# Kernel tuning notes

Hardware: AMD Instinct MI355X
Metric: run time of the kernel (lower is better)

## Reference

```python
import jax, jax.numpy as jnp
import numpy as np
from jax import lax

B, C, H, W = 8, 64, 256, 256
WSIZES = [8, 8]
DRATES = [1, 2]
SHIFT = True
CS = C // len(WSIZES)          # split channels = 32
SCALE = CS ** (-0.5)
EPS = 1e-6


def _ln2d(x, w, b):
    # channel-wise LayerNorm over dim 1 (biased variance), per LayerNormFunction
    mu = x.mean(1, keepdims=True)
    var = ((x - mu) ** 2).mean(1, keepdims=True)
    y = (x - mu) / jnp.sqrt(var + EPS)
    return w[None, :, None, None] * y + b[None, :, None, None]


def _conv1d(x, w, pad, dil):
    # x: [b, ci, L], w: [co, ci, k]
    return lax.conv_general_dilated(x, w, (1,), ((pad, pad),), rhs_dilation=(dil,),
                                    dimension_numbers=('NCH', 'OIH', 'NCH'))


def _eca(x, w1, w2, w3, wc):
    # x: [b,c,h,w] -> channel attention [b,c,1,1]
    y = x.mean((2, 3))[:, None, :]                      # [b,1,c]
    y1 = _conv1d(y, w1, 1, 1)
    y2 = _conv1d(y, w2, 2, 2)
    y3 = _conv1d(y, w3, 4, 4)
    y = _conv1d(jnp.concatenate([y1, y2, y3], axis=1), wc, 1, 1)  # [b,1,c]
    return jax.nn.sigmoid(jnp.transpose(y, (0, 2, 1))[..., None])  # [b,c,1,1]


def _conv1x1(x, w):
    # w: [co, ci]
    return jnp.einsum('bchw,oc->bohw', x, w)


def _win(x, ws):
    # [b,c,H,W] -> [(b nh nw), ws*ws, c]
    b, c, h, w = x.shape
    nh, nw = h // ws, w // ws
    x = x.reshape(b, c, nh, ws, nw, ws).transpose(0, 2, 4, 3, 5, 1)
    return x.reshape(b * nh * nw, ws * ws, c)


def _unwin(x, b, nh, nw, ws):
    c = x.shape[-1]
    x = x.reshape(b, nh, nw, ws, ws, c).transpose(0, 5, 1, 3, 2, 4)
    return x.reshape(b, c, nh * ws, nw * ws)


def setup_inputs() -> dict:
    key = jax.random.key(0)
    ks = jax.random.split(key, 16)
    g = lambda k, shape: jax.random.normal(k, shape, jnp.float32) * 0.02
    return {
        'x0': jax.random.normal(ks[0], (B, C, H, W), jnp.float32),
        'ln_w': jnp.ones((C,), jnp.float32),
        'ln_b': jnp.zeros((C,), jnp.float32),
        'dw_w': g(ks[1], (C, 1, 3, 3)),
        'dw_b': jnp.zeros((C,), jnp.float32),
        'eca_w1': g(ks[2], (1, 1, 3)),
        'eca_w2': g(ks[3], (1, 1, 3)),
        'eca_w3': g(ks[4], (1, 1, 3)),
        'eca_wc': g(ks[5], (1, 3, 3)),
        'wq': g(ks[6], (C, C)),
        'wk': g(ks[7], (C, C)),
        'wv': g(ks[8], (C, C)),
        'down_w': g(ks[9], (CS, 1, 2, 2)),
        'down_b': jnp.zeros((CS,), jnp.float32),
        'sa_w': g(ks[10], (1, C)),
        'sa_b': jnp.zeros((1,), jnp.float32),
        'po_w': g(ks[11], (C, C)),
        'po_b': jnp.zeros((C,), jnp.float32),
    }


def reference(x0, ln_w, ln_b, dw_w, dw_b, eca_w1, eca_w2, eca_w3, eca_wc,
              wq, wk, wv, down_w, down_b, sa_w, sa_b, po_w, po_b):
    b, c, h, w = x0.shape
    x = _ln2d(x0, ln_w, ln_b)
    # depthwise 3x3
    x1 = lax.conv_general_dilated(x, dw_w, (1, 1), ((1, 1), (1, 1)),
                                  feature_group_count=c,
                                  dimension_numbers=('NCHW', 'OIHW', 'NCHW'))
    x1 = x1 + dw_b[None, :, None, None]
    ca = _eca(x1, eca_w1, eca_w2, eca_w3, eca_wc)
    vs = jnp.split(_conv1x1(x, wv) * ca, len(WSIZES), axis=1)
    qs = jnp.split(_conv1x1(x, wq), len(WSIZES), axis=1)
    ks_ = jnp.split(_conv1x1(x, wk), len(WSIZES), axis=1)

    ys = []
    for idx in range(len(WSIZES)):
        ws = WSIZES[idx]
        ds = ws // DRATES[idx]
        q = qs[idx]
        if SHIFT:
            q = jnp.roll(q, (-ws // 2, -ws // 2), (2, 3))
        q = _win(q, ws)
        if DRATES[idx] != 1:
            # depthwise 2x2 stride-2 downsample of k, v
            def down(t):
                t = lax.conv_general_dilated(t, down_w, (2, 2), 'VALID',
                                             feature_group_count=CS,
                                             dimension_numbers=('NCHW', 'OIHW', 'NCHW'))
                return t + down_b[None, :, None, None]
            k = down(ks_[idx])
            v = down(vs[idx])
            if SHIFT:
                k = jnp.roll(k, (-ds // 2, -ds // 2), (2, 3))
                v = jnp.roll(v, (-ds // 2, -ds // 2), (2, 3))
            k = _win(k, ds)
            v = _win(v, ds)
        else:
            k, v = ks_[idx], vs[idx]
            if SHIFT:
                k = jnp.roll(k, (-ws // 2, -ws // 2), (2, 3))
                v = jnp.roll(v, (-ws // 2, -ws // 2), (2, 3))
            k = _win(k, ws)
            v = _win(v, ws)
        atn = jax.nn.softmax(jnp.einsum('nqc,nkc->nqk', q, k) * SCALE, axis=-1)
        y_ = jnp.einsum('nqk,nkc->nqc', atn, v)
        y_ = _unwin(y_, b, h // ws, w // ws, ws)
        if SHIFT:
            y_ = jnp.roll(y_, (ws // 2, ws // 2), (2, 3))
        ys.append(y_)

    y = jnp.concatenate(ys, axis=1)
    x1m = jax.nn.sigmoid(_conv1x1(y, sa_w) + sa_b[None, :, None, None]) * x1
    y = _conv1x1(y + x1m, po_w) + po_b[None, :, None, None]
    return y + x0
```

## Files before the change

### kernel.cpp

```cpp
#include <hip/hip_runtime.h>
#include <hip/hip_bf16.h>

using bf16 = __hip_bfloat16;

constexpr int B = 8, C = 64, H = 256, W = 256;
constexpr int HWs = H * W;
constexpr int NPIX = B * H * W;
constexpr long long NELEM = (long long)B * C * H * W;
constexpr int CS = 32;
constexpr int Hd = 128, Wd = 128;
constexpr int HWd = Hd * Wd;
constexpr int NDOWN = B * CS * HWd;
constexpr float EPS = 1e-6f;
constexpr float SCALE = 0.17677669529663687f;

typedef __attribute__((ext_vector_type(8))) short short8v;
typedef __attribute__((ext_vector_type(8))) unsigned short ushort8v;
typedef __attribute__((ext_vector_type(4))) unsigned short ushort4v;
typedef __attribute__((ext_vector_type(4))) float f32x4;

__device__ __forceinline__ float b2f(bf16 v) { return __bfloat162float(v); }
__device__ __forceinline__ bf16 f2b(float v) { return __float2bfloat16(v); }
__device__ __forceinline__ unsigned short f2bu(float v) {
  bf16 t = __float2bfloat16(v);
  unsigned short u;
  __builtin_memcpy(&u, &t, 2);
  return u;
}
__device__ __forceinline__ float bu2f(unsigned short u) {
  bf16 t;
  __builtin_memcpy(&t, &u, 2);
  return __bfloat162float(t);
}
__device__ __forceinline__ short8v pack2(ushort4v a, ushort4v b) {
  short8v r;
  r[0] = (short)a[0]; r[1] = (short)a[1]; r[2] = (short)a[2]; r[3] = (short)a[3];
  r[4] = (short)b[0]; r[5] = (short)b[1]; r[6] = (short)b[2]; r[7] = (short)b[3];
  return r;
}

__global__ __launch_bounds__(256) void qkv_ln_kernel(
    const float* __restrict__ x0, const float* __restrict__ lnw,
    const float* __restrict__ lnb, const float* __restrict__ wq,
    const float* __restrict__ wk, const float* __restrict__ wv,
    unsigned short* __restrict__ xo, unsigned short* __restrict__ q0,
    unsigned short* __restrict__ q1, unsigned short* __restrict__ k0,
    unsigned short* __restrict__ v0, unsigned short* __restrict__ ksp,
    unsigned short* __restrict__ vsp) {
  __shared__ unsigned short zs[4][16 * 80];
  int lane = threadIdx.x & 63, wid = threadIdx.x >> 6;
  int lr = lane & 15, lg = lane >> 4;
  short8v aq[4][2], ak[4][2], av[4][2];
#pragma unroll
  for (int mt = 0; mt < 4; ++mt)
#pragma unroll
    for (int ks = 0; ks < 2; ++ks) {
      int rowoff = (mt * 16 + lr) * 64 + ks * 32 + lg * 4;
      short8v tq, tk, tv;
#pragma unroll
      for (int j = 0; j < 8; ++j) {
        int kj = (j & 3) + 16 * (j >> 2);
        tq[j] = (short)f2bu(wq[rowoff + kj]);
        tk[j] = (short)f2bu(wk[rowoff + kj]);
        tv[j] = (short)f2bu(wv[rowoff + kj]);
      }
      aq[mt][ks] = tq; ak[mt][ks] = tk; av[mt][ks] = tv;
    }
  float lwv[16], lbv[16];
#pragma unroll
  for (int ks = 0; ks < 2; ++ks)
#pragma unroll
    for (int j = 0; j < 8; ++j) {
      int c = ks * 32 + lg * 4 + (j & 3) + 16 * (j >> 2);
      lwv[ks * 8 + j] = lnw[c];
      lbv[ks * 8 + j] = lnb[c];
    }
  unsigned short* slab = &zs[wid][0];
  const int NT = NPIX / 16;
  for (int t = blockIdx.x * 4 + wid; t < NT; t += gridDim.x * 4) {
    int p0 = t * 16;
    int b = p0 >> 16;
    int hw0 = p0 & (HWs - 1);
    const float* xp = x0 + (size_t)b * C * HWs + hw0 + lr;
    float xv[16];
#pragma unroll
    for (int ks = 0; ks < 2; ++ks)
#pragma unroll
      for (int j = 0; j < 8; ++j) {
        int c = ks * 32 + lg * 4 + (j & 3) + 16 * (j >> 2);
        xv[ks * 8 + j] = xp[(size_t)c * HWs];
      }
    float s = 0.f, s2 = 0.f;
#pragma unroll
    for (int i = 0; i < 16; ++i) { s += xv[i]; s2 += xv[i] * xv[i]; }
    s += __shfl_xor(s, 16, 64); s += __shfl_xor(s, 32, 64);
    s2 += __shfl_xor(s2, 16, 64); s2 += __shfl_xor(s2, 32, 64);
    float mu = s * (1.f / 64);
    float var = s2 * (1.f / 64) - mu * mu;
    float rstd = rsqrtf(var + EPS);
    short8v bx[2];
#pragma unroll
    for (int ks = 0; ks < 2; ++ks)
#pragma unroll
      for (int j = 0; j < 8; ++j) {
        float xn = lwv[ks * 8 + j] * ((xv[ks * 8 + j] - mu) * rstd) + lbv[ks * 8 + j];
        bx[ks][j] = (short)f2bu(xn);
      }
    int r = hw0 >> 8, col0 = hw0 & 255;
    int rr = (r - 4) & 255;
    int tokr = (rr & 7) * 8;
    int wrow = b * 1024 + (rr >> 3) * 32;
    int px = lane & 15, ch4 = lane >> 4;
    int ccw = (col0 + px - 4) & 255;
    size_t wb = (size_t)(wrow + (ccw >> 3)) * 2048 + (size_t)(tokr + (ccw & 7)) * 32 + ch4 * 8;
    int chs = 32 + (lane & 31), ph = lane >> 5;
    f32x4 zero = {0.f, 0.f, 0.f, 0.f};
#pragma unroll
    for (int ks = 0; ks < 2; ++ks)
#pragma unroll
      for (int j = 0; j < 8; ++j) {
        int c = ks * 32 + lg * 4 + (j & 3) + 16 * (j >> 2);
        slab[lr * 80 + c] = (unsigned short)bx[ks][j];
      }
    {
      int ch = lane;
      ushort8v d0, d1;
#pragma unroll
      for (int j2 = 0; j2 < 8; ++j2) {
        d0[j2] = slab[j2 * 80 + ch];
        d1[j2] = slab[(8 + j2) * 80 + ch];
      }
      size_t sb = ((size_t)b * 64 + ch) * HWs + hw0;
      *(ushort8v*)(xo + sb) = d0;
      *(ushort8v*)(xo + sb + 8) = d1;
    }
    {
      f32x4 acc[4];
#pragma unroll
      for (int mt = 0; mt < 4; ++mt) {
        acc[mt] = __builtin_amdgcn_mfma_f32_16x16x32_bf16(aq[mt][0], bx[0], zero, 0, 0, 0);
        acc[mt] = __builtin_amdgcn_mfma_f32_16x16x32_bf16(aq[mt][1], bx[1], acc[mt], 0, 0, 0);
      }
#pragma unroll
      for (int mt = 0; mt < 4; ++mt)
#pragma unroll
        for (int i = 0; i < 4; ++i)
          slab[lr * 80 + mt * 16 + lg * 4 + i] = f2bu(acc[mt][i]);
      ushort8v dq0 = *(const ushort8v*)&slab[px * 80 + ch4 * 8];
      ushort8v dq1 = *(const ushort8v*)&slab[px * 80 + 32 + ch4 * 8];
      *(ushort8v*)(q0 + wb) = dq0;
      *(ushort8v*)(q1 + wb) = dq1;
    }
    {
      f32x4 acc[4];
#pragma unroll
      for (int mt = 0; mt < 4; ++mt) {
        acc[mt] = __builtin_amdgcn_mfma_f32_16x16x32_bf16(ak[mt][0], bx[0], zero, 0, 0, 0);
        acc[mt] = __builtin_amdgcn_mfma_f32_16x16x32_bf16(ak[mt][1], bx[1], acc[mt], 0, 0, 0);
      }
#pragma unroll
      for (int mt = 0; mt < 4; ++mt)
#pragma unroll
        for (int i = 0; i < 4; ++i)
          slab[lr * 80 + mt * 16 + lg * 4 + i] = f2bu(acc[mt][i]);
      ushort8v dk = *(const ushort8v*)&slab[px * 80 + ch4 * 8];
      *(ushort8v*)(k0 + wb) = dk;
      ushort8v dks;
#pragma unroll
      for (int j2 = 0; j2 < 8; ++j2) dks[j2] = slab[(ph * 8 + j2) * 80 + chs];
      size_t sb = ((size_t)b * 32 + (chs - 32)) * HWs + hw0 + ph * 8;
      *(ushort8v*)(ksp + sb) = dks;
    }
    {
      f32x4 acc[4];
#pragma unroll
      for (int mt = 0; mt < 4; ++mt) {
        acc[mt] = __builtin_amdgcn_mfma_f32_16x16x32_bf16(av[mt][0], bx[0], zero, 0, 0, 0);
        acc[mt] = __builtin_amdgcn_mfma_f32_16x16x32_bf16(av[mt][1], bx[1], acc[mt], 0, 0, 0);
      }
#pragma unroll
      for (int mt = 0; mt < 4; ++mt)
#pragma unroll
        for (int i = 0; i < 4; ++i)
          slab[lr * 80 + mt * 16 + lg * 4 + i] = f2bu(acc[mt][i]);
      ushort8v dv = *(const ushort8v*)&slab[px * 80 + ch4 * 8];
      *(ushort8v*)(v0 + wb) = dv;
      ushort8v dvs;
#pragma unroll
      for (int j2 = 0; j2 < 8; ++j2) dvs[j2] = slab[(ph * 8 + j2) * 80 + chs];
      size_t sb = ((size_t)b * 32 + (chs - 32)) * HWs + hw0 + ph * 8;
      *(ushort8v*)(vsp + sb) = dvs;
    }
  }
}

__global__ __launch_bounds__(256) void dw_kernel(
    const unsigned short* __restrict__ x, const float* __restrict__ dww,
    const float* __restrict__ dwb, unsigned short* __restrict__ x1,
    float* __restrict__ pool) {
  int tid = threadIdx.x;
  int tx = tid & 15, ty = tid >> 4;
  int h = blockIdx.x * 16 + ty;
  int c = blockIdx.y, b = blockIdx.z;
  const unsigned short* xp = x + ((size_t)b * C + c) * HWs;
  float kk[9];
#pragma unroll
  for (int i = 0; i < 9; ++i) kk[i] = dww[c * 9 + i];
  int w0 = tx * 16;
  float acc[16];
  float bias = dwb[c];
#pragma unroll
  for (int i = 0; i < 16; ++i) acc[i] = bias;
#pragma unroll
  for (int dr = 0; dr < 3; ++dr) {
    int hh = h + dr - 1;
    if (hh < 0 || hh >= H) continue;
    const unsigned short* rp = xp + hh * W;
    ushort8v r0 = *(const ushort8v*)(rp + w0);
    ushort8v r1 = *(const ushort8v*)(rp + w0 + 8);
    float p[18];
    p[0] = (w0 > 0) ? bu2f(rp[w0 - 1]) : 0.f;
    p[17] = (w0 + 16 < W) ? bu2f(rp[w0 + 16]) : 0.f;
#pragma unroll
    for (int i = 0; i < 8; ++i) { p[1 + i] = bu2f(r0[i]); p[9 + i] = bu2f(r1[i]); }
    float k0 = kk[dr * 3], k1 = kk[dr * 3 + 1], k2 = kk[dr * 3 + 2];
#pragma unroll
    for (int i = 0; i < 16; ++i)
      acc[i] += k0 * p[i] + k1 * p[i + 1] + k2 * p[i + 2];
  }
  ushort8v o0, o1;
  float s = 0.f;
#pragma unroll
  for (int i = 0; i < 8; ++i) { o0[i] = f2bu(acc[i]); o1[i] = f2bu(acc[i + 8]); }
#pragma unroll
  for (int i = 0; i < 16; ++i) s += acc[i];
  size_t ob = ((size_t)b * C + c) * HWs + h * W + w0;
  *(ushort8v*)(x1 + ob) = o0;
  *(ushort8v*)(x1 + ob + 8) = o1;
#pragma unroll
  for (int off = 32; off > 0; off >>= 1) s += __shfl_down(s, off, 64);
  __shared__ float red[4];
  if ((tid & 63) == 0) red[tid >> 6] = s;
  __syncthreads();
  if (tid == 0) atomicAdd(&pool[b * C + c], red[0] + red[1] + red[2] + red[3]);
}

__global__ __launch_bounds__(512) void eca_kernel(
    const float* __restrict__ pool, const float* __restrict__ w1,
    const float* __restrict__ w2, const float* __restrict__ w3,
    const float* __restrict__ wc, float* __restrict__ ca) {
  int tid = threadIdx.x;
  int b = tid >> 6, c = tid & 63;
  __shared__ float m[8][64], t1[8][64], t2[8][64], t3[8][64];
  m[b][c] = pool[tid] * (1.f / HWs);
  __syncthreads();
  auto gm = [&](int cc) -> float { return (cc >= 0 && cc < 64) ? m[b][cc] : 0.f; };
  t1[b][c] = w1[0] * gm(c - 1) + w1[1] * gm(c) + w1[2] * gm(c + 1);
  t2[b][c] = w2[0] * gm(c - 2) + w2[1] * gm(c) + w2[2] * gm(c + 2);
  t3[b][c] = w3[0] * gm(c - 4) + w3[1] * gm(c) + w3[2] * gm(c + 4);
  __syncthreads();
  auto g1 = [&](int cc) -> float { return (cc >= 0 && cc < 64) ? t1[b][cc] : 0.f; };
  auto g2 = [&](int cc) -> float { return (cc >= 0 && cc < 64) ? t2[b][cc] : 0.f; };
  auto g3 = [&](int cc) -> float { return (cc >= 0 && cc < 64) ? t3[b][cc] : 0.f; };
  float z = 0.f;
#pragma unroll
  for (int k = 0; k < 3; ++k) {
    z += wc[0 * 3 + k] * g1(c + k - 1);
    z += wc[1 * 3 + k] * g2(c + k - 1);
    z += wc[2 * 3 + k] * g3(c + k - 1);
  }
  ca[tid] = 1.f / (1.f + __expf(-z));
}

__global__ __launch_bounds__(256) void down_kernel(
    const unsigned short* __restrict__ ksp, const unsigned short* __restrict__ vsp,
    const float* __restrict__ dw, const float* __restrict__ db,
    unsigned short* __restrict__ kdw, unsigned short* __restrict__ vdw) {
  int t = blockIdx.x * 256 + threadIdx.x;
  int wxd = t & 31, i = (t >> 5) & 127, c = (t >> 12) & 31, b = t >> 17;
  const unsigned short* kp = ksp + ((size_t)b * 32 + c) * HWs;
  const unsigned short* vp = vsp + ((size_t)b * 32 + c) * HWs;
  float w00 = dw[c * 4], w01 = dw[c * 4 + 1], w10 = dw[c * 4 + 2], w11 = dw[c * 4 + 3];
  float bias = db[c];
  int rowa = (2 * i) * W, rowb = rowa + W;
  int c0a = (8 * wxd + 4) & 255, c0b = (8 * wxd + 8) & 255;
  ushort4v ka0 = *(const ushort4v*)(kp + rowa + c0a);
  ushort4v ka1 = *(const ushort4v*)(kp + rowa + c0b);
  ushort4v kb0 = *(const ushort4v*)(kp + rowb + c0a);
  ushort4v kb1 = *(const ushort4v*)(kp + rowb + c0b);
  ushort4v va0 = *(const ushort4v*)(vp + rowa + c0a);
  ushort4v va1 = *(const ushort4v*)(vp + rowa + c0b);
  ushort4v vb0 = *(const ushort4v*)(vp + rowb + c0a);
  ushort4v vb1 = *(const ushort4v*)(vp + rowb + c0b);
  int rr = (i - 2) & 127;
  size_t winb = ((size_t)(b * 1024 + (rr >> 2) * 32 + wxd)) * 512;
  int tokrow = (rr & 3) * 4;
  ushort4v hk, hv;
#pragma unroll
  for (int tx = 0; tx < 4; ++tx) {
    float k00, k01, k10, k11, v00, v01, v10, v11;
    if (tx < 2) {
      k00 = bu2f(ka0[2 * tx]); k01 = bu2f(ka0[2 * tx + 1]);
      k10 = bu2f(kb0[2 * tx]); k11 = bu2f(kb0[2 * tx + 1]);
      v00 = bu2f(va0[2 * tx]); v01 = bu2f(va0[2 * tx + 1]);
      v10 = bu2f(vb0[2 * tx]); v11 = bu2f(vb0[2 * tx + 1]);
    } else {
      k00 = bu2f(ka1[2 * (tx - 2)]); k01 = bu2f(ka1[2 * (tx - 2) + 1]);
      k10 = bu2f(kb1[2 * (tx - 2)]); k11 = bu2f(kb1[2 * (tx - 2) + 1]);
      v00 = bu2f(va1[2 * (tx - 2)]); v01 = bu2f(va1[2 * (tx - 2) + 1]);
      v10 = bu2f(vb1[2 * (tx - 2)]); v11 = bu2f(vb1[2 * (tx - 2) + 1]);
    }
    hk[tx] = f2bu(w00 * k00 + w01 * k01 + w10 * k10 + w11 * k11 + bias);
    hv[tx] = f2bu(w00 * v00 + w01 * v01 + w10 * v10 + w11 * v11 + bias);
  }
  *(ushort4v*)(vdw + winb + (size_t)c * 16 + tokrow) = hv;
#pragma unroll
  for (int tx = 0; tx < 4; ++tx)
    kdw[winb + (size_t)(tokrow + tx) * 32 + c] = hk[tx];
}

__global__ __launch_bounds__(256) void attn0_kernel(
    const unsigned short* __restrict__ q0, const unsigned short* __restrict__ k0,
    const unsigned short* __restrict__ v0, const float* __restrict__ ca,
    unsigned short* __restrict__ y) {
  __shared__ unsigned short zs[4][32][72];
  int lane = threadIdx.x & 63, wid = threadIdx.x >> 6;
  int lr = lane & 15, lg = lane >> 4;
  int widx = blockIdx.x * 4 + wid;
  int b = widx >> 10, wy = (widx >> 5) & 31, wx = widx & 31;
  unsigned short* zw = &zs[wid][0][0];
  float cav[8];
#pragma unroll
  for (int mt = 0; mt < 2; ++mt)
#pragma unroll
    for (int r2 = 0; r2 < 4; ++r2)
      cav[mt * 4 + r2] = ca[b * 64 + mt * 16 + lg * 4 + r2];
  {
    const unsigned short* vp = v0 + (size_t)widx * 2048 + (size_t)lane * 32;
#pragma unroll
    for (int j2 = 0; j2 < 4; ++j2) {
      ushort8v vv = *(const ushort8v*)(vp + j2 * 8);
#pragma unroll
      for (int i = 0; i < 8; ++i) zw[(j2 * 8 + i) * 72 + lane] = vv[i];
    }
  }
  const unsigned short* kw = k0 + (size_t)widx * 2048;
  const unsigned short* qw = q0 + (size_t)widx * 2048;
  short8v kf[4], qf[4];
#pragma unroll
  for (int kt = 0; kt < 4; ++kt) {
    ushort4v a = *(const ushort4v*)(kw + (kt * 16 + lr) * 32 + lg * 4);
    ushort4v b2 = *(const ushort4v*)(kw + (kt * 16 + lr) * 32 + lg * 4 + 16);
    kf[kt] = pack2(a, b2);
  }
#pragma unroll
  for (int qt = 0; qt < 4; ++qt) {
    ushort4v a = *(const ushort4v*)(qw + (qt * 16 + lr) * 32 + lg * 4);
    ushort4v b2 = *(const ushort4v*)(qw + (qt * 16 + lr) * 32 + lg * 4 + 16);
    qf[qt] = pack2(a, b2);
  }
  __syncthreads();
  short8v va[2][2];
#pragma unroll
  for (int mt = 0; mt < 2; ++mt)
#pragma unroll
    for (int ck = 0; ck < 2; ++ck) {
      ushort4v a = *(const ushort4v*)&zw[(mt * 16 + lr) * 72 + ck * 32 + lg * 4];
      ushort4v b2 = *(const ushort4v*)&zw[(mt * 16 + lr) * 72 + ck * 32 + lg * 4 + 16];
      va[mt][ck] = pack2(a, b2);
    }
  f32x4 zero = {0.f, 0.f, 0.f, 0.f};
#pragma unroll
  for (int qt = 0; qt < 4; ++qt) {
    f32x4 st[4];
#pragma unroll
    for (int kt = 0; kt < 4; ++kt)
      st[kt] = __builtin_amdgcn_mfma_f32_16x16x32_bf16(kf[kt], qf[qt], zero, 0, 0, 0);
    float mx = -1e30f;
#pragma unroll
    for (int kt = 0; kt < 4; ++kt)
#pragma unroll
      for (int r2 = 0; r2 < 4; ++r2) mx = fmaxf(mx, st[kt][r2]);
    mx = fmaxf(mx, __shfl_xor(mx, 16, 64));
    mx = fmaxf(mx, __shfl_xor(mx, 32, 64));
    float sum = 0.f;
#pragma unroll
    for (int kt = 0; kt < 4; ++kt)
#pragma unroll
      for (int r2 = 0; r2 < 4; ++r2) {
        float e = __expf(SCALE * (st[kt][r2] - mx));
        st[kt][r2] = e;
        sum += e;
      }
    sum += __shfl_xor(sum, 16, 64);
    sum += __shfl_xor(sum, 32, 64);
    float inv = 1.f / sum;
    short8v pb[2];
#pragma unroll
    for (int ck = 0; ck < 2; ++ck)
#pragma unroll
      for (int j = 0; j < 8; ++j)
        pb[ck][j] = (short)f2bu(st[ck * 2 + (j >> 2)][j & 3]);
#pragma unroll
    for (int mt = 0; mt < 2; ++mt) {
      f32x4 yt = __builtin_amdgcn_mfma_f32_16x16x32_bf16(va[mt][0], pb[0], zero, 0, 0, 0);
      yt = __builtin_amdgcn_mfma_f32_16x16x32_bf16(va[mt][1], pb[1], yt, 0, 0, 0);
#pragma unroll
      for (int r2 = 0; r2 < 4; ++r2)
        zw[(mt * 16 + lg * 4 + r2) * 72 + qt * 16 + lr] = f2bu(yt[r2] * inv * cav[mt * 4 + r2]);
    }
  }
  __syncthreads();
  int ch = lane & 31, rh = lane >> 5;
  size_t ybase = ((size_t)b * C + ch) * HWs;
  int c1 = wx * 8 + 4, c2 = (wx * 8 + 8) & 255;
#pragma unroll
  for (int k2 = 0; k2 < 4; ++k2) {
    int row = rh * 4 + k2;
    ushort8v t8 = *(const ushort8v*)&zw[ch * 72 + row * 8];
    int r = (wy * 8 + row + 4) & 255;
    ushort4v lo, hi;
#pragma unroll
    for (int i = 0; i < 4; ++i) { lo[i] = t8[i]; hi[i] = t8[4 + i]; }
    *(ushort4v*)(y + ybase + r * W + c1) = lo;
    *(ushort4v*)(y + ybase + r * W + c2) = hi;
  }
}

__global__ __launch_bounds__(256) void attn1_kernel(
    const unsigned short* __restrict__ q1, const unsigned short* __restrict__ kdw,
    const unsigned short* __restrict__ vdw, const float* __restrict__ ca,
    unsigned short* __restrict__ y) {
  __shared__ unsigned short zs[4][32][72];
  int lane = threadIdx.x & 63, wid = threadIdx.x >> 6;
  int lr = lane & 15, lg = lane >> 4;
  int widx = blockIdx.x * 4 + wid;
  int b = widx >> 10, wy = (widx >> 5) & 31, wx = widx & 31;
  unsigned short* zw = &zs[wid][0][0];
  float cav[8];
#pragma unroll
  for (int mt = 0; mt < 2; ++mt)
#pragma unroll
    for (int r2 = 0; r2 < 4; ++r2)
      cav[mt * 4 + r2] = ca[b * 64 + 32 + mt * 16 + lg * 4 + r2];
  short8v kfr;
  {
    ushort4v a = *(const ushort4v*)(kdw + (size_t)widx * 512 + lr * 32 + lg * 4);
    ushort4v b2 = *(const ushort4v*)(kdw + (size_t)widx * 512 + lr * 32 + lg * 4 + 16);
    kfr = pack2(a, b2);
  }
  short8v va[2];
#pragma unroll
  for (int mt = 0; mt < 2; ++mt) {
    ushort4v a = *(const ushort4v*)(vdw + (size_t)widx * 512 + (mt * 16 + lr) * 16 + lg * 4);
    short8v t;
#pragma unroll
    for (int i = 0; i < 4; ++i) { t[i] = (short)a[i]; t[4 + i] = 0; }
    va[mt] = t;
  }
  const unsigned short* qw = q1 + (size_t)widx * 2048;
  short8v qf[4];
#pragma unroll
  for (int qt = 0; qt < 4; ++qt) {
    ushort4v a = *(const ushort4v*)(qw + (qt * 16 + lr) * 32 + lg * 4);
    ushort4v b2 = *(const ushort4v*)(qw + (qt * 16 + lr) * 32 + lg * 4 + 16);
    qf[qt] = pack2(a, b2);
  }
  f32x4 zero = {0.f, 0.f, 0.f, 0.f};
#pragma unroll
  for (int qt = 0; qt < 4; ++qt) {
    f32x4 st = __builtin_amdgcn_mfma_f32_16x16x32_bf16(kfr, qf[qt], zero, 0, 0, 0);
    float mx = fmaxf(fmaxf(st[0], st[1]), fmaxf(st[2], st[3]));
    mx = fmaxf(mx, __shfl_xor(mx, 16, 64));
    mx = fmaxf(mx, __shfl_xor(mx, 32, 64));
    float sum = 0.f;
#pragma unroll
    for (int r2 = 0; r2 < 4; ++r2) {
      float e = __expf(SCALE * (st[r2] - mx));
      st[r2] = e;
      sum += e;
    }
    sum += __shfl_xor(sum, 16, 64);
    sum += __shfl_xor(sum, 32, 64);
    float inv = 1.f / sum;
    short8v pb;
#pragma unroll
    for (int j = 0; j < 4; ++j) { pb[j] = (short)f2bu(st[j]); pb[4 + j] = 0; }
#pragma unroll
    for (int mt = 0; mt < 2; ++mt) {
      f32x4 yt = __builtin_amdgcn_mfma_f32_16x16x32_bf16(va[mt], pb, zero, 0, 0, 0);
#pragma unroll
      for (int r2 = 0; r2 < 4; ++r2)
        zw[(mt * 16 + lg * 4 + r2) * 72 + qt * 16 + lr] = f2bu(yt[r2] * inv * cav[mt * 4 + r2]);
    }
  }
  __syncthreads();
  int ch = lane & 31, rh = lane >> 5;
  size_t ybase = ((size_t)b * C + 32 + ch) * HWs;
  int c1 = wx * 8 + 4, c2 = (wx * 8 + 8) & 255;
#pragma unroll
  for (int k2 = 0; k2 < 4; ++k2) {
    int row = rh * 4 + k2;
    ushort8v t8 = *(const ushort8v*)&zw[ch * 72 + row * 8];
    int r = (wy * 8 + row + 4) & 255;
    ushort4v lo, hi;
#pragma unroll
    for (int i = 0; i < 4; ++i) { lo[i] = t8[i]; hi[i] = t8[4 + i]; }
    *(ushort4v*)(y + ybase + r * W + c1) = lo;
    *(ushort4v*)(y + ybase + r * W + c2) = hi;
  }
}

__global__ __launch_bounds__(256) void final_mfma_kernel(
    const unsigned short* __restrict__ y, const unsigned short* __restrict__ x1,
    const float* __restrict__ x0, const float* __restrict__ sa_w,
    const float* __restrict__ sa_b, const float* __restrict__ po_w,
    const float* __restrict__ po_b, float* __restrict__ out) {
  __shared__ unsigned short zs[64][72];
  __shared__ float part[4][64];
  __shared__ float sgs[64];
  int tid = threadIdx.x;
  int lane = tid & 63, wid = tid >> 6;
  int lr = lane & 15, lg = lane >> 4;
  short8v ap[4][2];
#pragma unroll
  for (int mt = 0; mt < 4; ++mt)
#pragma unroll
    for (int ks = 0; ks < 2; ++ks) {
      int rowoff = (mt * 16 + lr) * 64 + ks * 32 + lg * 4;
      short8v tt;
#pragma unroll
      for (int j = 0; j < 8; ++j) {
        int kj = (j & 3) + 16 * (j >> 2);
        tt[j] = (short)f2bu(po_w[rowoff + kj]);
      }
      ap[mt][ks] = tt;
    }
  int cc = tid >> 2, qx = (tid & 3) * 16;
  const int NBLK = NPIX / 64;
  for (int blk = blockIdx.x; blk < NBLK; blk += gridDim.x) {
    int p0 = blk * 64;
    int b = p0 >> 16, hw0 = p0 & (HWs - 1);
    size_t rbase = (size_t)b * C * HWs + (size_t)cc * HWs + hw0 + qx;
    ushort8v y0 = *(const ushort8v*)(y + rbase);
    ushort8v y1 = *(const ushort8v*)(y + rbase + 8);
    ushort8v a0 = *(const ushort8v*)(x1 + rbase);
    ushort8v a1 = *(const ushort8v*)(x1 + rbase + 8);
    *(ushort8v*)&zs[cc][qx] = y0;
    *(ushort8v*)&zs[cc][qx + 8] = y1;
    __syncthreads();
    {
      int p = tid & 63, qr = tid >> 6;
      float s = 0.f;
#pragma unroll
      for (int c2 = 0; c2 < 16; ++c2)
        s += sa_w[qr * 16 + c2] * bu2f(zs[qr * 16 + c2][p]);
      part[qr][p] = s;
    }
    __syncthreads();
    if (tid < 64) {
      float sd = part[0][tid] + part[1][tid] + part[2][tid] + part[3][tid] + sa_b[0];
      sgs[tid] = 1.f / (1.f + __expf(-sd));
    }
    __syncthreads();
    {
      ushort8v z0, z1;
#pragma unroll
      for (int i = 0; i < 8; ++i) {
        z0[i] = f2bu(bu2f(y0[i]) + sgs[qx + i] * bu2f(a0[i]));
        z1[i] = f2bu(bu2f(y1[i]) + sgs[qx + 8 + i] * bu2f(a1[i]));
      }
      *(ushort8v*)&zs[cc][qx] = z0;
      *(ushort8v*)&zs[cc][qx + 8] = z1;
    }
    __syncthreads();
    short8v bz[2];
#pragma unroll
    for (int ks = 0; ks < 2; ++ks) {
      short8v tt;
#pragma unroll
      for (int j = 0; j < 8; ++j) {
        int c2 = ks * 32 + lg * 4 + (j & 3) + 16 * (j >> 2);
        tt[j] = (short)zs[c2][wid * 16 + lr];
      }
      bz[ks] = tt;
    }
    f32x4 zero = {0.f, 0.f, 0.f, 0.f};
    f32x4 acc[4];
#pragma unroll
    for (int mt = 0; mt < 4; ++mt) {
      acc[mt] = __builtin_amdgcn_mfma_f32_16x16x32_bf16(ap[mt][0], bz[0], zero, 0, 0, 0);
      acc[mt] = __builtin_amdgcn_mfma_f32_16x16x32_bf16(ap[mt][1], bz[1], acc[mt], 0, 0, 0);
    }
    size_t pbase = (size_t)b * C * HWs + hw0 + wid * 16 + lr;
#pragma unroll
    for (int mt = 0; mt < 4; ++mt)
#pragma unroll
      for (int i = 0; i < 4; ++i) {
        int o = mt * 16 + lg * 4 + i;
        out[pbase + (size_t)o * HWs] = acc[mt][i] + po_b[o] + x0[pbase + (size_t)o * HWs];
      }
    __syncthreads();
  }
}

extern "C" void kernel_launch(void* const* d_in, const int* in_sizes, int n_in,
                              void* d_out, int out_size, void* d_ws, size_t ws_size,
                              hipStream_t stream) {
  const float* x0    = (const float*)d_in[0];
  const float* ln_w  = (const float*)d_in[1];
  const float* ln_b  = (const float*)d_in[2];
  const float* dw_w  = (const float*)d_in[3];
  const float* dw_b  = (const float*)d_in[4];
  const float* ew1   = (const float*)d_in[5];
  const float* ew2   = (const float*)d_in[6];
  const float* ew3   = (const float*)d_in[7];
  const float* ewc   = (const float*)d_in[8];
  const float* wq    = (const float*)d_in[9];
  const float* wk    = (const float*)d_in[10];
  const float* wv    = (const float*)d_in[11];
  const float* dwn_w = (const float*)d_in[12];
  const float* dwn_b = (const float*)d_in[13];
  const float* sa_w  = (const float*)d_in[14];
  const float* sa_b  = (const float*)d_in[15];
  const float* po_w  = (const float*)d_in[16];
  const float* po_b  = (const float*)d_in[17];
  float* out = (float*)d_out;

  char* ws = (char*)d_ws;
  const size_t NB = (size_t)NELEM * sizeof(bf16);
  const size_t NH = NB / 2;
  const size_t NDB = (size_t)NDOWN * sizeof(bf16);
  bf16* xbuf  = (bf16*)(ws);
  bf16* x1buf = (bf16*)(ws + NB);
  unsigned short* q0b  = (unsigned short*)(ws + 2 * NB);
  unsigned short* q1b  = (unsigned short*)(ws + 2 * NB + NH);
  unsigned short* k0b  = (unsigned short*)(ws + 3 * NB);
  unsigned short* v0b  = (unsigned short*)(ws + 3 * NB + NH);
  unsigned short* kspb = (unsigned short*)(ws + 4 * NB);
  unsigned short* vspb = (unsigned short*)(ws + 4 * NB + NH);
  unsigned short* kdwb = (unsigned short*)(ws + 5 * NB);
  unsigned short* vdwb = (unsigned short*)(ws + 5 * NB + NDB);
  float* pool = (float*)(ws + 5 * NB + 2 * NDB);
  float* cabuf = pool + B * C;
  bf16* ybuf = xbuf;

  hipMemsetAsync(pool, 0, B * C * sizeof(float), stream);
  qkv_ln_kernel<<<2048, 256, 0, stream>>>(x0, ln_w, ln_b, wq, wk, wv,
                                          (unsigned short*)xbuf, q0b, q1b, k0b, v0b,
                                          kspb, vspb);
  dw_kernel<<<dim3(16, C, B), 256, 0, stream>>>((const unsigned short*)xbuf, dw_w, dw_b,
                                                (unsigned short*)x1buf, pool);
  eca_kernel<<<1, 512, 0, stream>>>(pool, ew1, ew2, ew3, ewc, cabuf);
  down_kernel<<<4096, 256, 0, stream>>>(kspb, vspb, dwn_w, dwn_b, kdwb, vdwb);
  attn0_kernel<<<2048, 256, 0, stream>>>(q0b, k0b, v0b, cabuf, (unsigned short*)ybuf);
  attn1_kernel<<<2048, 256, 0, stream>>>(q1b, kdwb, vdwb, cabuf, (unsigned short*)ybuf);
  final_mfma_kernel<<<2048, 256, 0, stream>>>((const unsigned short*)ybuf,
                                              (const unsigned short*)x1buf, x0,
                                              sa_w, sa_b, po_w, po_b, out);
}
```

Before: 407.4 us.

## Restructure QKV kernel into 64-pixel segments and coalesce attention output stores

The QKV/LayerNorm kernel stops using a grid-stride loop over 16-pixel tiles. Each wave now handles one 64-pixel segment, loading weight fragments one matrix at a time instead of holding all three, and stages outputs through two LDS buffers so that windowed and channel-major stores become wider and more contiguous. In both attention kernels the output store is now done cooperatively by the whole block across its four adjacent windows, giving 16-byte stores instead of split 8-byte ones. The aim is better global-store coalescing and lower register pressure, at the cost of more LDS traffic. The new kernel also relies on the launch grid covering exactly NPIX/64 segments.

```diff
diff --git a/kernel.cpp b/kernel.cpp
--- a/kernel.cpp
+++ b/kernel.cpp
@@ -47,25 +47,17 @@
     unsigned short* __restrict__ q1, unsigned short* __restrict__ k0,
     unsigned short* __restrict__ v0, unsigned short* __restrict__ ksp,
     unsigned short* __restrict__ vsp) {
-  __shared__ unsigned short zs[4][16 * 80];
+  __shared__ unsigned short sA[4][2560];
+  __shared__ unsigned short sB[4][2560];
   int lane = threadIdx.x & 63, wid = threadIdx.x >> 6;
   int lr = lane & 15, lg = lane >> 4;
-  short8v aq[4][2], ak[4][2], av[4][2];
-#pragma unroll
-  for (int mt = 0; mt < 4; ++mt)
-#pragma unroll
-    for (int ks = 0; ks < 2; ++ks) {
-      int rowoff = (mt * 16 + lr) * 64 + ks * 32 + lg * 4;
-      short8v tq, tk, tv;
-#pragma unroll
-      for (int j = 0; j < 8; ++j) {
-        int kj = (j & 3) + 16 * (j >> 2);
-        tq[j] = (short)f2bu(wq[rowoff + kj]);
-        tk[j] = (short)f2bu(wk[rowoff + kj]);
-        tv[j] = (short)f2bu(wv[rowoff + kj]);
-      }
-      aq[mt][ks] = tq; ak[mt][ks] = tk; av[mt][ks] = tv;
-    }
+  unsigned short* A = &sA[wid][0];
+  unsigned short* Bs = &sB[wid][0];
+  int seg = blockIdx.x * 4 + wid;
+  int p0 = seg * 64;
+  int b = p0 >> 16;
+  int hw0 = p0 & (HWs - 1);
+  int r = hw0 >> 8, col0 = hw0 & 255;
   float lwv[16], lbv[16];
 #pragma unroll
   for (int ks = 0; ks < 2; ++ks)
@@ -75,13 +67,10 @@
       lwv[ks * 8 + j] = lnw[c];
       lbv[ks * 8 + j] = lnb[c];
     }
-  unsigned short* slab = &zs[wid][0];
-  const int NT = NPIX / 16;
-  for (int t = blockIdx.x * 4 + wid; t < NT; t += gridDim.x * 4) {
-    int p0 = t * 16;
-    int b = p0 >> 16;
-    int hw0 = p0 & (HWs - 1);
-    const float* xp = x0 + (size_t)b * C * HWs + hw0 + lr;
+  short8v bx[4][2];
+#pragma unroll
+  for (int st = 0; st < 4; ++st) {
+    const float* xp = x0 + (size_t)b * C * HWs + hw0 + st * 16 + lr;
     float xv[16];
 #pragma unroll
     for (int ks = 0; ks < 2; ++ks)
@@ -98,98 +87,150 @@
     float mu = s * (1.f / 64);
     float var = s2 * (1.f / 64) - mu * mu;
     float rstd = rsqrtf(var + EPS);
-    short8v bx[2];
 #pragma unroll
     for (int ks = 0; ks < 2; ++ks)
 #pragma unroll
       for (int j = 0; j < 8; ++j) {
         float xn = lwv[ks * 8 + j] * ((xv[ks * 8 + j] - mu) * rstd) + lbv[ks * 8 + j];
-        bx[ks][j] = (short)f2bu(xn);
-      }
-    int r = hw0 >> 8, col0 = hw0 & 255;
-    int rr = (r - 4) & 255;
-    int tokr = (rr & 7) * 8;
-    int wrow = b * 1024 + (rr >> 3) * 32;
-    int px = lane & 15, ch4 = lane >> 4;
-    int ccw = (col0 + px - 4) & 255;
-    size_t wb = (size_t)(wrow + (ccw >> 3)) * 2048 + (size_t)(tokr + (ccw & 7)) * 32 + ch4 * 8;
-    int chs = 32 + (lane & 31), ph = lane >> 5;
-    f32x4 zero = {0.f, 0.f, 0.f, 0.f};
-#pragma unroll
-    for (int ks = 0; ks < 2; ++ks)
+        bx[st][ks][j] = (short)f2bu(xn);
+      }
+  }
+  int rr = (r - 4) & 255;
+  int tokr = (rr & 7) * 8;
+  int wrow = b * 1024 + (rr >> 3) * 32;
+  auto win_store = [&](const unsigned short* src, unsigned short* dst) {
+#pragma unroll
+    for (int i = 0; i < 4; ++i) {
+      int g = i * 4 + (lane >> 4);
+      int tl = (lane >> 2) & 3, ch8 = lane & 3;
+      int px = g * 4 + tl;
+      int ccw = (col0 + px - 4) & 255;
+      size_t wb = (size_t)(wrow + (ccw >> 3)) * 2048 +
+                  (size_t)(tokr + (ccw & 7)) * 32 + ch8 * 8;
+      ushort8v d = *(const ushort8v*)(src + px * 40 + ch8 * 8);
+      *(ushort8v*)(dst + wb) = d;
+    }
+  };
+  auto load_wfrag = [&](const float* wsrc, short8v wf[4][2]) {
+#pragma unroll
+    for (int mt = 0; mt < 4; ++mt)
+#pragma unroll
+      for (int ks = 0; ks < 2; ++ks) {
+        int rowoff = (mt * 16 + lr) * 64 + ks * 32 + lg * 4;
+        short8v t;
+#pragma unroll
+        for (int j = 0; j < 8; ++j) {
+          int kj = (j & 3) + 16 * (j >> 2);
+          t[j] = (short)f2bu(wsrc[rowoff + kj]);
+        }
+        wf[mt][ks] = t;
+      }
+  };
+  f32x4 zero = {0.f, 0.f, 0.f, 0.f};
+#pragma unroll
+  for (int half = 0; half < 2; ++half) {
+#pragma unroll
+    for (int st = 0; st < 4; ++st) {
+      int px = st * 16 + lr;
 #pragma unroll
       for (int j = 0; j < 8; ++j) {
-        int c = ks * 32 + lg * 4 + (j & 3) + 16 * (j >> 2);
-        slab[lr * 80 + c] = (unsigned short)bx[ks][j];
-      }
-    {
-      int ch = lane;
-      ushort8v d0, d1;
-#pragma unroll
-      for (int j2 = 0; j2 < 8; ++j2) {
-        d0[j2] = slab[j2 * 80 + ch];
-        d1[j2] = slab[(8 + j2) * 80 + ch];
-      }
-      size_t sb = ((size_t)b * 64 + ch) * HWs + hw0;
-      *(ushort8v*)(xo + sb) = d0;
-      *(ushort8v*)(xo + sb + 8) = d1;
-    }
-    {
+        int c = lg * 4 + (j & 3) + 16 * (j >> 2);
+        Bs[c * 80 + px] = (unsigned short)bx[st][half][j];
+      }
+    }
+#pragma unroll
+    for (int i = 0; i < 4; ++i) {
+      int ch = i * 8 + (lane >> 3), pxg = lane & 7;
+      ushort8v d = *(const ushort8v*)(Bs + ch * 80 + pxg * 8);
+      *(ushort8v*)(xo + ((size_t)b * 64 + half * 32 + ch) * HWs + hw0 + pxg * 8) = d;
+    }
+  }
+  {
+    short8v wf[4][2];
+    load_wfrag(wq, wf);
+#pragma unroll
+    for (int st = 0; st < 4; ++st) {
       f32x4 acc[4];
 #pragma unroll
       for (int mt = 0; mt < 4; ++mt) {
-        acc[mt] = __builtin_amdgcn_mfma_f32_16x16x32_bf16(aq[mt][0], bx[0], zero, 0, 0, 0);
-        acc[mt] = __builtin_amdgcn_mfma_f32_16x16x32_bf16(aq[mt][1], bx[1], acc[mt], 0, 0, 0);
-      }
-#pragma unroll
-      for (int mt = 0; mt < 4; ++mt)
+        acc[mt] = __builtin_amdgcn_mfma_f32_16x16x32_bf16(wf[mt][0], bx[st][0], zero, 0, 0, 0);
+        acc[mt] = __builtin_amdgcn_mfma_f32_16x16x32_bf16(wf[mt][1], bx[st][1], acc[mt], 0, 0, 0);
+      }
+      int px = st * 16 + lr;
+#pragma unroll
+      for (int mt = 0; mt < 2; ++mt)
 #pragma unroll
         for (int i = 0; i < 4; ++i)
-          slab[lr * 80 + mt * 16 + lg * 4 + i] = f2bu(acc[mt][i]);
-      ushort8v dq0 = *(const ushort8v*)&slab[px * 80 + ch4 * 8];
-      ushort8v dq1 = *(const ushort8v*)&slab[px * 80 + 32 + ch4 * 8];
-      *(ushort8v*)(q0 + wb) = dq0;
-      *(ushort8v*)(q1 + wb) = dq1;
-    }
-    {
+          A[px * 40 + mt * 16 + lg * 4 + i] = f2bu(acc[mt][i]);
+#pragma unroll
+      for (int mt = 2; mt < 4; ++mt)
+#pragma unroll
+        for (int i = 0; i < 4; ++i)
+          Bs[px * 40 + (mt - 2) * 16 + lg * 4 + i] = f2bu(acc[mt][i]);
+    }
+    win_store(A, q0);
+    win_store(Bs, q1);
+  }
+  {
+    short8v wf[4][2];
+    load_wfrag(wk, wf);
+#pragma unroll
+    for (int st = 0; st < 4; ++st) {
       f32x4 acc[4];
 #pragma unroll
       for (int mt = 0; mt < 4; ++mt) {
-        acc[mt] = __builtin_amdgcn_mfma_f32_16x16x32_bf16(ak[mt][0], bx[0], zero, 0, 0, 0);
-        acc[mt] = __builtin_amdgcn_mfma_f32_16x16x32_bf16(ak[mt][1], bx[1], acc[mt], 0, 0, 0);
-      }
-#pragma unroll
-      for (int mt = 0; mt < 4; ++mt)
+        acc[mt] = __builtin_amdgcn_mfma_f32_16x16x32_bf16(wf[mt][0], bx[st][0], zero, 0, 0, 0);
+        acc[mt] = __builtin_amdgcn_mfma_f32_16x16x32_bf16(wf[mt][1], bx[st][1], acc[mt], 0, 0, 0);
+      }
+      int px = st * 16 + lr;
+#pragma unroll
+      for (int mt = 0; mt < 2; ++mt)
 #pragma unroll
         for (int i = 0; i < 4; ++i)
-          slab[lr * 80 + mt * 16 + lg * 4 + i] = f2bu(acc[mt][i]);
-      ushort8v dk = *(const ushort8v*)&slab[px * 80 + ch4 * 8];
-      *(ushort8v*)(k0 + wb) = dk;
-      ushort8v dks;
-#pragma unroll
-      for (int j2 = 0; j2 < 8; ++j2) dks[j2] = slab[(ph * 8 + j2) * 80 + chs];
-      size_t sb = ((size_t)b * 32 + (chs - 32)) * HWs + hw0 + ph * 8;
-      *(ushort8v*)(ksp + sb) = dks;
-    }
-    {
+          A[px * 40 + mt * 16 + lg * 4 + i] = f2bu(acc[mt][i]);
+#pragma unroll
+      for (int mt = 2; mt < 4; ++mt)
+#pragma unroll
+        for (int i = 0; i < 4; ++i)
+          Bs[((mt - 2) * 16 + lg * 4 + i) * 80 + px] = f2bu(acc[mt][i]);
+    }
+    win_store(A, k0);
+#pragma unroll
+    for (int i = 0; i < 4; ++i) {
+      int ch = i * 8 + (lane >> 3), pxg = lane & 7;
+      ushort8v d = *(const ushort8v*)(Bs + ch * 80 + pxg * 8);
+      *(ushort8v*)(ksp + ((size_t)b * 32 + ch) * HWs + hw0 + pxg * 8) = d;
+    }
+  }
+  {
+    short8v wf[4][2];
+    load_wfrag(wv, wf);
+#pragma unroll
+    for (int st = 0; st < 4; ++st) {
       f32x4 acc[4];
 #pragma unroll
       for (int mt = 0; mt < 4; ++mt) {
-        acc[mt] = __builtin_amdgcn_mfma_f32_16x16x32_bf16(av[mt][0], bx[0], zero, 0, 0, 0);
-        acc[mt] = __builtin_amdgcn_mfma_f32_16x16x32_bf16(av[mt][1], bx[1], acc[mt], 0, 0, 0);
-      }
-#pragma unroll
-      for (int mt = 0; mt < 4; ++mt)
+        acc[mt] = __builtin_amdgcn_mfma_f32_16x16x32_bf16(wf[mt][0], bx[st][0], zero, 0, 0, 0);
+        acc[mt] = __builtin_amdgcn_mfma_f32_16x16x32_bf16(wf[mt][1], bx[st][1], acc[mt], 0, 0, 0);
+      }
+      int px = st * 16 + lr;
+#pragma unroll
+      for (int mt = 0; mt < 2; ++mt)
 #pragma unroll
         for (int i = 0; i < 4; ++i)
-          slab[lr * 80 + mt * 16 + lg * 4 + i] = f2bu(acc[mt][i]);
-      ushort8v dv = *(const ushort8v*)&slab[px * 80 + ch4 * 8];
-      *(ushort8v*)(v0 + wb) = dv;
-      ushort8v dvs;
-#pragma unroll
-      for (int j2 = 0; j2 < 8; ++j2) dvs[j2] = slab[(ph * 8 + j2) * 80 + chs];
-      size_t sb = ((size_t)b * 32 + (chs - 32)) * HWs + hw0 + ph * 8;
-      *(ushort8v*)(vsp + sb) = dvs;
+          A[px * 40 + mt * 16 + lg * 4 + i] = f2bu(acc[mt][i]);
+#pragma unroll
+      for (int mt = 2; mt < 4; ++mt)
+#pragma unroll
+        for (int i = 0; i < 4; ++i)
+          Bs[((mt - 2) * 16 + lg * 4 + i) * 80 + px] = f2bu(acc[mt][i]);
+    }
+    win_store(A, v0);
+#pragma unroll
+    for (int i = 0; i < 4; ++i) {
+      int ch = i * 8 + (lane >> 3), pxg = lane & 7;
+      ushort8v d = *(const ushort8v*)(Bs + ch * 80 + pxg * 8);
+      *(ushort8v*)(vsp + ((size_t)b * 32 + ch) * HWs + hw0 + pxg * 8) = d;
     }
   }
 }
@@ -324,10 +365,11 @@
     const unsigned short* __restrict__ v0, const float* __restrict__ ca,
     unsigned short* __restrict__ y) {
   __shared__ unsigned short zs[4][32][72];
-  int lane = threadIdx.x & 63, wid = threadIdx.x >> 6;
+  int tid = threadIdx.x;
+  int lane = tid & 63, wid = tid >> 6;
   int lr = lane & 15, lg = lane >> 4;
   int widx = blockIdx.x * 4 + wid;
-  int b = widx >> 10, wy = (widx >> 5) & 31, wx = widx & 31;
+  int b = widx >> 10;
   unsigned short* zw = &zs[wid][0][0];
   float cav[8];
 #pragma unroll
@@ -411,19 +453,26 @@
     }
   }
   __syncthreads();
-  int ch = lane & 31, rh = lane >> 5;
-  size_t ybase = ((size_t)b * C + ch) * HWs;
-  int c1 = wx * 8 + 4, c2 = (wx * 8 + 8) & 255;
-#pragma unroll
-  for (int k2 = 0; k2 < 4; ++k2) {
-    int row = rh * 4 + k2;
-    ushort8v t8 = *(const ushort8v*)&zw[ch * 72 + row * 8];
-    int r = (wy * 8 + row + 4) & 255;
-    ushort4v lo, hi;
-#pragma unroll
-    for (int i = 0; i < 4; ++i) { lo[i] = t8[i]; hi[i] = t8[4 + i]; }
-    *(ushort4v*)(y + ybase + r * W + c1) = lo;
-    *(ushort4v*)(y + ybase + r * W + c2) = hi;
+  int widx0 = blockIdx.x * 4;
+  int b0 = widx0 >> 10, wy0 = (widx0 >> 5) & 31, wxb = widx0 & 31;
+#pragma unroll
+  for (int pass = 0; pass < 4; ++pass) {
+    int sub = tid & 3, pair = tid >> 2;
+    int ch = pair & 31;
+    int row = pass * 2 + (pair >> 5);
+    ushort8v t8 = *(const ushort8v*)&zs[sub][ch][row * 8];
+    int r2 = (wy0 * 8 + row + 4) & 255;
+    int colb = wxb * 8 + 4 + sub * 8;
+    size_t yb = ((size_t)b0 * C + ch) * HWs + (size_t)r2 * W;
+    if (colb <= 248) {
+      *(ushort8v*)(y + yb + colb) = t8;
+    } else {
+      ushort4v lo, hi;
+#pragma unroll
+      for (int i = 0; i < 4; ++i) { lo[i] = t8[i]; hi[i] = t8[4 + i]; }
+      *(ushort4v*)(y + yb + 252) = lo;
+      *(ushort4v*)(y + yb) = hi;
+    }
   }
 }
 
@@ -432,10 +481,11 @@
     const unsigned short* __restrict__ vdw, const float* __restrict__ ca,
     unsigned short* __restrict__ y) {
   __shared__ unsigned short zs[4][32][72];
-  int lane = threadIdx.x & 63, wid = threadIdx.x >> 6;
+  int tid = threadIdx.x;
+  int lane = tid & 63, wid = tid >> 6;
   int lr = lane & 15, lg = lane >> 4;
   int widx = blockIdx.x * 4 + wid;
-  int b = widx >> 10, wy = (widx >> 5) & 31, wx = widx & 31;
+  int b = widx >> 10;
   unsigned short* zw = &zs[wid][0][0];
   float cav[8];
 #pragma unroll
@@ -495,19 +545,26 @@
     }
   }
   __syncthreads();
-  int ch = lane & 31, rh = lane >> 5;
-  size_t ybase = ((size_t)b * C + 32 + ch) * HWs;
-  int c1 = wx * 8 + 4, c2 = (wx * 8 + 8) & 255;
-#pragma unroll
-  for (int k2 = 0; k2 < 4; ++k2) {
-    int row = rh * 4 + k2;
-    ushort8v t8 = *(const ushort8v*)&zw[ch * 72 + row * 8];
-    int r = (wy * 8 + row + 4) & 255;
-    ushort4v lo, hi;
-#pragma unroll
-    for (int i = 0; i < 4; ++i) { lo[i] = t8[i]; hi[i] = t8[4 + i]; }
-    *(ushort4v*)(y + ybase + r * W + c1) = lo;
-    *(ushort4v*)(y + ybase + r * W + c2) = hi;
+  int widx0 = blockIdx.x * 4;
+  int b0 = widx0 >> 10, wy0 = (widx0 >> 5) & 31, wxb = widx0 & 31;
+#pragma unroll
+  for (int pass = 0; pass < 4; ++pass) {
+    int sub = tid & 3, pair = tid >> 2;
+    int ch = pair & 31;
+    int row = pass * 2 + (pair >> 5);
+    ushort8v t8 = *(const ushort8v*)&zs[sub][ch][row * 8];
+    int r2 = (wy0 * 8 + row + 4) & 255;
+    int colb = wxb * 8 + 4 + sub * 8;
+    size_t yb = ((size_t)b0 * C + 32 + ch) * HWs + (size_t)r2 * W;
+    if (colb <= 248) {
+      *(ushort8v*)(y + yb + colb) = t8;
+    } else {
+      ushort4v lo, hi;
+#pragma unroll
+      for (int i = 0; i < 4; ++i) { lo[i] = t8[i]; hi[i] = t8[4 + i]; }
+      *(ushort4v*)(y + yb + 252) = lo;
+      *(ushort4v*)(y + yb) = hi;
+    }
   }
 }
 
```

New measurement: 343.2 us, median of 2. 1.19x faster.
